# Kernel optimization log

Measured on AMD Instinct MI355X. Metric: run time of the kernel, lower is better.

Reference implementation:

```python
import jax, jax.numpy as jnp
import numpy as np

N = 100000   # nodes
E = 1000000  # edges
DIN = 128    # atom_in_features
DE = 16      # edge_attr_dim
H = 128      # hidden width (preprocess/cheb/postprocess)
K = 3        # Chebyshev order
EPS = 1e-5


def setup_inputs() -> dict:
    key = jax.random.key(0)
    ks = jax.random.split(key, 16)
    s = 0.02
    return {
        "x": jax.random.normal(ks[0], (N, DIN), jnp.float32),
        "edge_index": jax.random.randint(ks[1], (2, E), 0, N),
        "edge_attr": jax.random.normal(ks[2], (E, DE), jnp.float32),
        # AtomEdgeInteraction linear: (DIN+DE) -> H
        "w_int": jax.random.normal(ks[3], (DIN + DE, H), jnp.float32) * s,
        "b_int": jnp.zeros((H,), jnp.float32),
        # preprocess layer 1: Linear + BatchNorm + ReLU
        "w_pre": jax.random.normal(ks[4], (H, H), jnp.float32) * s,
        "b_pre": jnp.zeros((H,), jnp.float32),
        "g_pre": jnp.ones((H,), jnp.float32),
        "be_pre": jnp.zeros((H,), jnp.float32),
        # ChebConv layers: weight [K, in, out] + bias
        "cheb1_w": jax.random.normal(ks[5], (K, H, H), jnp.float32) * s,
        "cheb1_b": jnp.zeros((H,), jnp.float32),
        "cheb2_w": jax.random.normal(ks[6], (K, H, H), jnp.float32) * s,
        "cheb2_b": jnp.zeros((H,), jnp.float32),
        # postprocess: Linear + BatchNorm + ReLU
        "w_post": jax.random.normal(ks[7], (H, H), jnp.float32) * s,
        "b_post": jnp.zeros((H,), jnp.float32),
        "g_post": jnp.ones((H,), jnp.float32),
        "be_post": jnp.zeros((H,), jnp.float32),
        # output layer H -> 1
        "w_out": jax.random.normal(ks[8], (H, 1), jnp.float32) * s,
        "b_out": jnp.zeros((1,), jnp.float32),
    }


def _bn(z, g, b):
    # BatchNorm1d, training-mode batch statistics (biased variance, like torch)
    m = z.mean(0)
    v = ((z - m) ** 2).mean(0)
    return g * (z - m) * jax.lax.rsqrt(v + EPS) + b


def _cheb(h, W, b, row, col, norm):
    # ChebConv with sym normalization, lambda_max=2 => L_hat = -D^{-1/2} A D^{-1/2}
    def lhat(z):
        return jax.ops.segment_sum(norm[:, None] * z[row], col, num_segments=N)

    Tx0 = h
    out = Tx0 @ W[0]
    Tx1 = lhat(Tx0)
    out = out + Tx1 @ W[1]
    for k in range(2, W.shape[0]):
        Tx2 = 2.0 * lhat(Tx1) - Tx0
        out = out + Tx2 @ W[k]
        Tx0, Tx1 = Tx1, Tx2
    return out + b


def reference(x, edge_index, edge_attr,
              w_int, b_int,
              w_pre, b_pre, g_pre, be_pre,
              cheb1_w, cheb1_b, cheb2_w, cheb2_b,
              w_post, b_post, g_post, be_post,
              w_out, b_out):
    row, col = edge_index[0], edge_index[1]
    ones_e = jnp.ones((E,), x.dtype)

    # AtomEdgeInteraction: gather -> concat -> linear -> scatter_mean over col
    comb = jnp.concatenate([x[row], edge_attr], axis=-1)  # [E, DIN+DE]
    upd = comb @ w_int + b_int                             # [E, H]
    cnt = jax.ops.segment_sum(ones_e, col, num_segments=N)
    h = jax.ops.segment_sum(upd, col, num_segments=N) / jnp.clip(cnt, 1.0)[:, None]

    # preprocess layer 1 (Linear + BN + ReLU; dropout rate 0)
    h = jax.nn.relu(_bn(h @ w_pre + b_pre, g_pre, be_pre))

    # sym-normalized edge coefficients for scaled Laplacian
    deg = jax.ops.segment_sum(ones_e, row, num_segments=N)
    dis = jnp.where(deg > 0, jax.lax.rsqrt(jnp.maximum(deg, 1.0)), 0.0)
    norm = -dis[row] * dis[col]  # [E]

    h = jax.nn.relu(_cheb(h, cheb1_w, cheb1_b, row, col, norm))
    h = jax.nn.relu(_cheb(h, cheb2_w, cheb2_b, row, col, norm))

    # postprocess (Linear + BN + ReLU)
    h = jax.nn.relu(_bn(h @ w_post + b_post, g_post, be_post))

    # output layer, squeeze(-1) -> [N]
    return (h @ w_out + b_out).squeeze(-1)
```

## Files before the change

kernel.cpp:

```cpp
#include <hip/hip_runtime.h>
#include <hip/hip_bf16.h>

using u16 = unsigned short;
using u32 = unsigned int;

#define NN 100000
#define NE 1000000
#define NBKT 196
#define NBLK 489

typedef __attribute__((ext_vector_type(8))) short bfrag;
typedef __attribute__((ext_vector_type(4))) float ffrag;

#define BF16ONE2 0x3F803F80u

__device__ __forceinline__ float bf2f(u16 u) { return __uint_as_float(((u32)u) << 16); }
__device__ __forceinline__ u16 f2bf(float f) {
  u32 x = __float_as_uint(f);
  return (u16)((x + 0x7fffu + ((x >> 16) & 1u)) >> 16);
}
__device__ __forceinline__ float rdv(const void* p, long i, int f) {
  return f ? bf2f(((const u16*)p)[i]) : ((const float*)p)[i];
}
__device__ __forceinline__ void acc8(float* a, uint4 v, float w) {
  a[0] = fmaf(w, __uint_as_float(v.x << 16), a[0]);
  a[1] = fmaf(w, __uint_as_float(v.x & 0xffff0000u), a[1]);
  a[2] = fmaf(w, __uint_as_float(v.y << 16), a[2]);
  a[3] = fmaf(w, __uint_as_float(v.y & 0xffff0000u), a[3]);
  a[4] = fmaf(w, __uint_as_float(v.z << 16), a[4]);
  a[5] = fmaf(w, __uint_as_float(v.z & 0xffff0000u), a[5]);
  a[6] = fmaf(w, __uint_as_float(v.w << 16), a[6]);
  a[7] = fmaf(w, __uint_as_float(v.w & 0xffff0000u), a[7]);
}
__device__ __forceinline__ void acc8bn(float* a, uint4 v, float w, const float* A,
                                       const float* Bb) {
  float x;
  x = __uint_as_float(v.x << 16);
  a[0] = fmaf(w, fmaxf(fmaf(A[0], x, Bb[0]), 0.f), a[0]);
  x = __uint_as_float(v.x & 0xffff0000u);
  a[1] = fmaf(w, fmaxf(fmaf(A[1], x, Bb[1]), 0.f), a[1]);
  x = __uint_as_float(v.y << 16);
  a[2] = fmaf(w, fmaxf(fmaf(A[2], x, Bb[2]), 0.f), a[2]);
  x = __uint_as_float(v.y & 0xffff0000u);
  a[3] = fmaf(w, fmaxf(fmaf(A[3], x, Bb[3]), 0.f), a[3]);
  x = __uint_as_float(v.z << 16);
  a[4] = fmaf(w, fmaxf(fmaf(A[4], x, Bb[4]), 0.f), a[4]);
  x = __uint_as_float(v.z & 0xffff0000u);
  a[5] = fmaf(w, fmaxf(fmaf(A[5], x, Bb[5]), 0.f), a[5]);
  x = __uint_as_float(v.w << 16);
  a[6] = fmaf(w, fmaxf(fmaf(A[6], x, Bb[6]), 0.f), a[6]);
  x = __uint_as_float(v.w & 0xffff0000u);
  a[7] = fmaf(w, fmaxf(fmaf(A[7], x, Bb[7]), 0.f), a[7]);
}

#define OWXT 0
#define OWPRE 16384
#define OWD1 32768
#define OW11 49152
#define OV21 65536
#define OWD2 81920
#define OW12 98304
#define OV22 114688
#define OWPOST 131072
#define OWET 147456

#define ASTRIDE 136
#define ESTRIDE 132

struct PrepArgs { const void* in[16]; };

__global__ void k_prep(PrepArgs a, const u32* __restrict__ gp, u16* __restrict__ wq,
                       float* __restrict__ wf) {
  int t = blockIdx.x * 256 + threadIdx.x;
  int f = (gp[0] == BF16ONE2) ? 1 : 0;
  if (t < 16384) {
    int o = t >> 7, k = t & 127;
    int ko = k * 128 + o;
    int ok = o * 128 + k;
    wq[OWXT + ok] = f2bf(rdv(a.in[0], ko, f));
    wq[OWPRE + ok] = f2bf(rdv(a.in[2], ko, f));
    float c0 = rdv(a.in[6], ko, f);
    float c1 = rdv(a.in[6], 16384 + ko, f);
    float c2 = rdv(a.in[6], 32768 + ko, f);
    wq[OWD1 + ok] = f2bf(c0 - c2);
    wq[OW11 + ok] = f2bf(c1);
    wq[OV21 + ok] = f2bf(2.f * c2);
    float d0 = rdv(a.in[8], ko, f);
    float d1 = rdv(a.in[8], 16384 + ko, f);
    float d2 = rdv(a.in[8], 32768 + ko, f);
    wq[OWD2 + ok] = f2bf(d0 - d2);
    wq[OW12 + ok] = f2bf(d1);
    wq[OV22 + ok] = f2bf(2.f * d2);
    wq[OWPOST + ok] = f2bf(rdv(a.in[10], ko, f));
  }
  if (t < 4096) {
    int o = t >> 5, k = t & 31;
    wq[OWET + o * 32 + k] = (k < 16) ? f2bf(rdv(a.in[0], (long)(128 + k) * 128 + o, f)) : (u16)0;
  }
  if (t < 1281) {
    int s = t >> 7, j = t & 127;
    const int map[11] = {1, 3, 4, 5, 7, 9, 11, 12, 13, 14, 15};
    wf[t] = rdv(a.in[map[s]], j, f);
  }
}


__global__ void k_cnt(const int* __restrict__ ei, int* __restrict__ bcnt,
                      int* __restrict__ rbcnt) {
  __shared__ int hc[NBKT], hr[NBKT];
  int t = threadIdx.x, blk = blockIdx.x;
  for (int i = t; i < NBKT; i += 256) { hc[i] = 0; hr[i] = 0; }
  __syncthreads();
  long base = (long)blk * 2048;
#pragma unroll
  for (int i = 0; i < 8; i++) {
    long e = base + i * 256 + t;
    if (e < NE) {
      atomicAdd(&hc[ei[NE + e] >> 9], 1);
      atomicAdd(&hr[ei[e] >> 9], 1);
    }
  }
  __syncthreads();
  for (int i = t; i < NBKT; i += 256) {
    bcnt[i * NBLK + blk] = hc[i];
    rbcnt[i * NBLK + blk] = hr[i];
  }
}

__global__ void k_bscan(int* __restrict__ bcnt, int* __restrict__ rbcnt,
                        int* __restrict__ btot) {
  __shared__ int ss[256];
  int j = blockIdx.x, t = threadIdx.x;
  int* arr = ((j < NBKT) ? bcnt : rbcnt) + (j % NBKT) * NBLK;
  int a = (2 * t < NBLK) ? arr[2 * t] : 0;
  int b = (2 * t + 1 < NBLK) ? arr[2 * t + 1] : 0;
  ss[t] = a + b;
  __syncthreads();
  for (int st = 1; st < 256; st <<= 1) {
    int x = (t >= st) ? ss[t - st] : 0;
    __syncthreads();
    ss[t] += x;
    __syncthreads();
  }
  int base = ss[t] - a - b;
  if (2 * t < NBLK) arr[2 * t] = base;
  if (2 * t + 1 < NBLK) arr[2 * t + 1] = base + a;
  if (t == 255) btot[j] = ss[255];
}

__global__ void k_bbase(const int* __restrict__ btot, int* __restrict__ bbase,
                        int* __restrict__ rbbase, int* __restrict__ off) {
  __shared__ int ss[256];
  int t = threadIdx.x;
  int v = (t < NBKT) ? btot[t] : 0;
  ss[t] = v;
  __syncthreads();
  for (int st = 1; st < 256; st <<= 1) {
    int x = (t >= st) ? ss[t - st] : 0;
    __syncthreads();
    ss[t] += x;
    __syncthreads();
  }
  if (t < NBKT) bbase[t] = ss[t] - v;
  if (t == NBKT - 1) bbase[NBKT] = ss[t];
  __syncthreads();
  int v2 = (t < NBKT) ? btot[NBKT + t] : 0;
  ss[t] = v2;
  __syncthreads();
  for (int st = 1; st < 256; st <<= 1) {
    int x = (t >= st) ? ss[t - st] : 0;
    __syncthreads();
    ss[t] += x;
    __syncthreads();
  }
  if (t < NBKT) rbbase[t] = ss[t] - v2;
  if (t == NBKT - 1) rbbase[NBKT] = ss[t];
  if (t == 0) off[NN] = NE;
}

__global__ void k_scat(const int* __restrict__ ei, const int* __restrict__ bofs,
                       const int* __restrict__ rbofs, const int* __restrict__ bbase,
                       const int* __restrict__ rbbase, u32* __restrict__ sle,
                       u32* __restrict__ srow, u16* __restrict__ srl) {
  __shared__ int cc[NBKT], cr[NBKT], cbase[NBKT], rbase[NBKT];
  int t = threadIdx.x, blk = blockIdx.x;
  for (int i = t; i < NBKT; i += 256) {
    cc[i] = 0;
    cr[i] = 0;
    cbase[i] = bbase[i] + bofs[i * NBLK + blk];
    rbase[i] = rbbase[i] + rbofs[i * NBLK + blk];
  }
  __syncthreads();
  long base = (long)blk * 2048;
#pragma unroll
  for (int i = 0; i < 8; i++) {
    long e = base + i * 256 + t;
    if (e < NE) {
      int c = ei[NE + e], r = ei[e];
      int k1 = atomicAdd(&cc[c >> 9], 1);
      int d1 = cbase[c >> 9] + k1;
      sle[d1] = ((u32)(c & 511) << 20) | (u32)e;
      srow[d1] = (u32)r;
      int k2 = atomicAdd(&cr[r >> 9], 1);
      int d2 = rbase[r >> 9] + k2;
      srl[d2] = (u16)(r & 511);
    }
  }
}

__global__ void k_fine(const u32* __restrict__ sle, const u32* __restrict__ srow,
                       const int* __restrict__ bbase, int* __restrict__ off,
                       int2* __restrict__ cpk) {
  __shared__ u32 hist[512];
  __shared__ u32 ss[256];
  int t = threadIdx.x, b = blockIdx.x;
  hist[t] = 0;
  hist[t + 256] = 0;
  __syncthreads();
  int lo = bbase[b], hi = bbase[b + 1];
  for (int p = lo + t; p < hi; p += 256) atomicAdd(&hist[sle[p] >> 20], 1);
  __syncthreads();
  u32 a = hist[2 * t], bb = hist[2 * t + 1];
  ss[t] = a + bb;
  __syncthreads();
  for (int st = 1; st < 256; st <<= 1) {
    u32 x = (t >= st) ? ss[t - st] : 0;
    __syncthreads();
    ss[t] += x;
    __syncthreads();
  }
  u32 base = ss[t] - a - bb;
  u32 c0 = (u32)lo + base, c1 = (u32)lo + base + a;
  hist[2 * t] = c0;
  hist[2 * t + 1] = c1;
  int col0 = b * 512 + 2 * t, col1 = col0 + 1;
  if (col0 < NN) off[col0] = (int)c0;
  if (col1 < NN) off[col1] = (int)c1;
  __syncthreads();
  for (int p = lo + t; p < hi; p += 256) {
    u32 v = sle[p];
    u32 pos = atomicAdd(&hist[v >> 20], 1);
    cpk[pos] = make_int2((int)srow[p], (int)(v & 0xFFFFFu));
  }
}

__global__ void k_deg(const u16* __restrict__ srl, const int* __restrict__ rbbase,
                      int* __restrict__ deg) {
  __shared__ int hist[512];
  int t = threadIdx.x, b = blockIdx.x;
  hist[t] = 0;
  hist[t + 256] = 0;
  __syncthreads();
  int lo = rbbase[b], hi = rbbase[b + 1];
  for (int p = lo + t; p < hi; p += 256) atomicAdd(&hist[srl[p]], 1);
  __syncthreads();
  int n0 = b * 512 + t, n1 = n0 + 256;
  if (n0 < NN) deg[n0] = hist[t];
  if (n1 < NN) deg[n1] = hist[t + 256];
}

template <int BN>
__global__ __launch_bounds__(256) void k_spmm(const u16* __restrict__ src,
                                              u16* __restrict__ dst,
                                              const int* __restrict__ off,
                                              const int2* __restrict__ cpk,
                                              const float* __restrict__ cnorm,
                                              const float* __restrict__ ab) {
  int t = threadIdx.x;
  int node = blockIdx.x * 8 + (t >> 5);
  if (node >= NN) return;
  int l = t & 31;
  int half = l >> 4;
  int c = (l & 15) * 8;
  float A[8], Bb[8];
  if (BN) {
#pragma unroll
    for (int j = 0; j < 8; j++) {
      A[j] = ab[c + j];
      Bb[j] = ab[128 + c + j];
    }
  }
  int p0 = off[node], p1 = off[node + 1];
  float a[8];
#pragma unroll
  for (int j = 0; j < 8; j++) a[j] = 0.f;
  const u16* sp = src + c;
  for (int p = p0 + half; p < p1; p += 8) {
    int rr[4];
    float w[4];
#pragma unroll
    for (int u = 0; u < 4; u++) {
      int q = p + u * 2;
      int qc = q < p1 ? q : p1 - 1;
      rr[u] = cpk[qc].x;
      w[u] = (q < p1) ? cnorm[qc] : 0.f;
    }
#pragma unroll
    for (int u = 0; u < 4; u++) {
      uint4 v = *(const uint4*)(sp + (long)rr[u] * 128);
      if (BN) acc8bn(a, v, w[u], A, Bb);
      else acc8(a, v, w[u]);
    }
  }
#pragma unroll
  for (int j = 0; j < 8; j++) a[j] += __shfl_xor(a[j], 16);
  if (half) return;
  uint4 o;
  o.x = (u32)f2bf(a[0]) | ((u32)f2bf(a[1]) << 16);
  o.y = (u32)f2bf(a[2]) | ((u32)f2bf(a[3]) << 16);
  o.z = (u32)f2bf(a[4]) | ((u32)f2bf(a[5]) << 16);
  o.w = (u32)f2bf(a[6]) | ((u32)f2bf(a[7]) << 16);
  *(uint4*)(dst + (long)node * 128 + c) = o;
}

template <int WEIGHTED>
__device__ __forceinline__ void gather_lds(u16* sA, const u16* __restrict__ src,
                                           const int* __restrict__ off,
                                           const int2* __restrict__ cpk,
                                           const float* __restrict__ cnorm, int r0) {
  int tid = threadIdx.x;
  int grp = tid >> 4;
  int c = (tid & 15) * 8;
  const u16* sp = src + c;
#pragma unroll
  for (int i = 0; i < 4; i++) {
    int nl = grp * 4 + i;
    int node = r0 + nl;
    float a[8];
#pragma unroll
    for (int j = 0; j < 8; j++) a[j] = 0.f;
    if (node < NN) {
      int p0 = off[node], p1 = off[node + 1];
      for (int p = p0; p < p1; p += 8) {
        int rr[8];
        float w[8];
#pragma unroll
        for (int u = 0; u < 8; u++) {
          int q = p + u;
          int qc = q < p1 ? q : p1 - 1;
          rr[u] = cpk[qc].x;
          w[u] = (q < p1) ? (WEIGHTED ? cnorm[qc] : 1.f) : 0.f;
        }
#pragma unroll
        for (int u = 0; u < 8; u++)
          acc8(a, *(const uint4*)(sp + (long)rr[u] * 128), w[u]);
      }
    }
    uint4 o;
    o.x = (u32)f2bf(a[0]) | ((u32)f2bf(a[1]) << 16);
    o.y = (u32)f2bf(a[2]) | ((u32)f2bf(a[3]) << 16);
    o.z = (u32)f2bf(a[4]) | ((u32)f2bf(a[5]) << 16);
    o.w = (u32)f2bf(a[6]) | ((u32)f2bf(a[7]) << 16);
    *(uint4*)(sA + nl * ASTRIDE + c) = o;
  }
}

__global__ __launch_bounds__(256) void k_asum(const void* __restrict__ eattr,
                                              const u32* __restrict__ gp,
                                              u16* __restrict__ asum,
                                              const int* __restrict__ off,
                                              const int2* __restrict__ cpk,
                                              const int* __restrict__ deg,
                                              float* __restrict__ cnorm) {
  int t = blockIdx.x * 256 + threadIdx.x;
  int node = t >> 4;
  if (node >= NN) return;
  int j = t & 15;
  int p0 = off[node], p1 = off[node + 1];
  int dn = deg[node];
  float ndis = dn > 0 ? -rsqrtf((float)dn) : 0.f;
  for (int p = p0 + j; p < p1; p += 16)
    cnorm[p] = ndis * rsqrtf((float)deg[cpk[p].x]);
  float a = 0.f;
  if (gp[0] == BF16ONE2) {
    const u16* e16 = (const u16*)eattr;
    for (int p = p0; p < p1; p += 8) {
      float s[8];
#pragma unroll
      for (int u = 0; u < 8; u++) {
        int q = p + u;
        int qc = q < p1 ? q : p1 - 1;
        float v = bf2f(e16[(long)cpk[qc].y * 16 + j]);
        s[u] = (q < p1) ? v : 0.f;
      }
      a += ((s[0] + s[1]) + (s[2] + s[3])) + ((s[4] + s[5]) + (s[6] + s[7]));
    }
  } else {
    const float* e32 = (const float*)eattr;
    for (int p = p0; p < p1; p += 8) {
      float s[8];
#pragma unroll
      for (int u = 0; u < 8; u++) {
        int q = p + u;
        int qc = q < p1 ? q : p1 - 1;
        float v = e32[(long)cpk[qc].y * 16 + j];
        s[u] = (q < p1) ? v : 0.f;
      }
      a += ((s[0] + s[1]) + (s[2] + s[3])) + ((s[4] + s[5]) + (s[6] + s[7]));
    }
  }
  asum[(long)node * 16 + j] = f2bf(a);
}

struct MArgs {
  const void* A0; const u16* W0T; int a0raw;
  const float* bias;
  u16* out;
  const u32* gp;
  float* part;
};

__global__ __launch_bounds__(256) void k_mgemm(MArgs m) {
  constexpr int ROWS = 128, RT = 8, TPR = 2, SEGW = 64;
  __shared__ __align__(16) u16 sA[ROWS * ASTRIDE];
  int tid = threadIdx.x;
  int wv = tid >> 6, lane = tid & 63;
  int col16 = lane & 15, quad = lane >> 4;
  int r0 = blockIdx.x * ROWS;

  ffrag acc[RT * 2];
#pragma unroll
  for (int i = 0; i < RT * 2; i++)
#pragma unroll
    for (int g = 0; g < 4; g++) acc[i][g] = 0.f;

  {
    int row = tid / TPR, seg = tid % TPR;
    int ra = r0 + row;
    if (ra >= NN) ra = NN - 1;
    bool f32a = m.a0raw && (m.gp[0] != BF16ONE2);
    if (f32a) {
      const float* gs = (const float*)m.A0 + (long)ra * 128 + seg * SEGW;
      u32* lp = (u32*)(sA + row * ASTRIDE + seg * SEGW);
#pragma unroll
      for (int e = 0; e < SEGW / 8; e++) {
        float4 v0 = *(const float4*)(gs + e * 8);
        float4 v1 = *(const float4*)(gs + e * 8 + 4);
        lp[e * 4 + 0] = (u32)f2bf(v0.x) | ((u32)f2bf(v0.y) << 16);
        lp[e * 4 + 1] = (u32)f2bf(v0.z) | ((u32)f2bf(v0.w) << 16);
        lp[e * 4 + 2] = (u32)f2bf(v1.x) | ((u32)f2bf(v1.y) << 16);
        lp[e * 4 + 3] = (u32)f2bf(v1.z) | ((u32)f2bf(v1.w) << 16);
      }
    } else {
      const u16* gs = (const u16*)m.A0 + (long)ra * 128 + seg * SEGW;
      uint4* lp = (uint4*)(sA + row * ASTRIDE + seg * SEGW);
#pragma unroll
      for (int e = 0; e < SEGW / 8; e++) lp[e] = *(const uint4*)(gs + e * 8);
    }
  }
  bfrag b0[2][4];
#pragma unroll
  for (int c = 0; c < 2; c++)
#pragma unroll
    for (int kb = 0; kb < 4; kb++)
      b0[c][kb] = *(const bfrag*)(m.W0T + (long)(wv * 32 + c * 16 + col16) * 128 + kb * 32 + quad * 8);
  __syncthreads();
#pragma unroll
  for (int kb = 0; kb < 4; kb++)
#pragma unroll
    for (int rt = 0; rt < RT; rt++) {
      bfrag af = *(const bfrag*)(sA + (rt * 16 + col16) * ASTRIDE + kb * 32 + quad * 8);
      acc[rt * 2 + 0] = __builtin_amdgcn_mfma_f32_16x16x32_bf16(af, b0[0][kb], acc[rt * 2 + 0], 0, 0, 0);
      acc[rt * 2 + 1] = __builtin_amdgcn_mfma_f32_16x16x32_bf16(af, b0[1][kb], acc[rt * 2 + 1], 0, 0, 0);
    }
  __syncthreads();
#pragma unroll
  for (int rt = 0; rt < RT; rt++)
#pragma unroll
    for (int c = 0; c < 2; c++) {
      int col = wv * 32 + c * 16 + col16;
      float bj = m.bias ? m.bias[col] : 0.f;
#pragma unroll
      for (int g = 0; g < 4; g++)
        sA[(rt * 16 + quad * 4 + g) * ESTRIDE + col] = f2bf(acc[rt * 2 + c][g] + bj);
    }
  __syncthreads();
  {
    int rr = tid / TPR, d = tid % TPR;
    int rowg = r0 + rr;
    if (rowg < NN) {
      const u16* sp2 = sA + rr * ESTRIDE + d * 64;
      uint4* o = (uint4*)(m.out + (long)rowg * 128 + d * 64);
#pragma unroll
      for (int e = 0; e < 8; e++) {
        const uint2* s2 = (const uint2*)(sp2 + e * 8);
        uint2 lo = s2[0], hi = s2[1];
        o[e] = make_uint4(lo.x, lo.y, hi.x, hi.y);
      }
    }
  }
  if (m.part) {
    __shared__ float ps[256], pq[256];
    int col = tid & 127, hf = tid >> 7;
    float s = 0.f, q = 0.f;
#pragma unroll
    for (int r = 0; r < 64; r++) {
      int rr = hf * 64 + r;
      if (r0 + rr < NN) {
        float v = bf2f(sA[rr * ESTRIDE + col]);
        s += v;
        q += v * v;
      }
    }
    ps[tid] = s;
    pq[tid] = q;
    __syncthreads();
    if (tid < 128) {
      m.part[(long)blockIdx.x * 256 + tid] = ps[tid] + ps[tid + 128];
      m.part[(long)blockIdx.x * 256 + 128 + tid] = pq[tid] + pq[tid + 128];
    }
  }
}

__global__ __launch_bounds__(256) void k_etpre(const u16* __restrict__ Xg,
                                               const u16* __restrict__ asum,
                                               const u16* __restrict__ Wet,
                                               const u16* __restrict__ Wpre,
                                               const float* __restrict__ b_int,
                                               const float* __restrict__ b_pre,
                                               const int* __restrict__ off,
                                               const int2* __restrict__ cpk,
                                               u16* __restrict__ out, float* part) {
  __shared__ __align__(16) u16 sA[64 * ASTRIDE];
  __shared__ __align__(16) u16 sE[64 * 32];
  int tid = threadIdx.x;
  int wv = tid >> 6, lane = tid & 63;
  int col16 = lane & 15, quad = lane >> 4;
  int r0 = blockIdx.x * 64;

  gather_lds<0>(sA, Xg, off, cpk, nullptr, r0);
  {
    int row = tid >> 2, seg = tid & 3;
    int ra = r0 + row;
    if (ra >= NN) ra = NN - 1;
    if (seg < 2)
      *(uint4*)(sE + row * 32 + seg * 8) = *(const uint4*)(asum + (long)ra * 16 + seg * 8);
    else
      *(uint4*)(sE + row * 32 + seg * 8) = make_uint4(0, 0, 0, 0);
  }
  bfrag be[2];
#pragma unroll
  for (int c = 0; c < 2; c++)
    be[c] = *(const bfrag*)(Wet + (long)(wv * 32 + c * 16 + col16) * 32 + quad * 8);
  __syncthreads();
  ffrag accE[8];
#pragma unroll
  for (int i = 0; i < 8; i++)
#pragma unroll
    for (int g = 0; g < 4; g++) accE[i][g] = 0.f;
#pragma unroll
  for (int rt = 0; rt < 4; rt++) {
    bfrag af = *(const bfrag*)(sE + (rt * 16 + col16) * 32 + quad * 8);
    accE[rt * 2 + 0] = __builtin_amdgcn_mfma_f32_16x16x32_bf16(af, be[0], accE[rt * 2 + 0], 0, 0, 0);
    accE[rt * 2 + 1] = __builtin_amdgcn_mfma_f32_16x16x32_bf16(af, be[1], accE[rt * 2 + 1], 0, 0, 0);
  }
#pragma unroll
  for (int rt = 0; rt < 4; rt++)
#pragma unroll
    for (int g = 0; g < 4; g++) {
      int rr = rt * 16 + quad * 4 + g;
      int r = r0 + rr;
      int cc = (r < NN) ? off[r + 1] - off[r] : 0;
      float inv = 1.f / (float)(cc > 1 ? cc : 1);
#pragma unroll
      for (int c = 0; c < 2; c++) {
        int col = wv * 32 + c * 16 + col16;
        float bj = b_int[col];
        float v = accE[rt * 2 + c][g] + bf2f(sA[rr * ASTRIDE + col]);
        v = (v + (float)cc * bj) * inv;
        sA[rr * ASTRIDE + col] = f2bf(v);
      }
    }
  bfrag b1[2][4];
#pragma unroll
  for (int c = 0; c < 2; c++)
#pragma unroll
    for (int kb = 0; kb < 4; kb++)
      b1[c][kb] = *(const bfrag*)(Wpre + (long)(wv * 32 + c * 16 + col16) * 128 + kb * 32 + quad * 8);
  __syncthreads();
  ffrag a2[8];
#pragma unroll
  for (int i = 0; i < 8; i++)
#pragma unroll
    for (int g = 0; g < 4; g++) a2[i][g] = 0.f;
#pragma unroll
  for (int kb = 0; kb < 4; kb++)
#pragma unroll
    for (int rt = 0; rt < 4; rt++) {
      bfrag af = *(const bfrag*)(sA + (rt * 16 + col16) * ASTRIDE + kb * 32 + quad * 8);
      a2[rt * 2 + 0] = __builtin_amdgcn_mfma_f32_16x16x32_bf16(af, b1[0][kb], a2[rt * 2 + 0], 0, 0, 0);
      a2[rt * 2 + 1] = __builtin_amdgcn_mfma_f32_16x16x32_bf16(af, b1[1][kb], a2[rt * 2 + 1], 0, 0, 0);
    }
  __syncthreads();
#pragma unroll
  for (int rt = 0; rt < 4; rt++)
#pragma unroll
    for (int c = 0; c < 2; c++) {
      int col = wv * 32 + c * 16 + col16;
      float bj = b_pre[col];
#pragma unroll
      for (int g = 0; g < 4; g++)
        sA[(rt * 16 + quad * 4 + g) * ESTRIDE + col] = f2bf(a2[rt * 2 + c][g] + bj);
    }
  __syncthreads();
  {
    int rr = tid >> 2, d = tid & 3;
    int rowg = r0 + rr;
    if (rowg < NN) {
      const u16* sp2 = sA + rr * ESTRIDE + d * 32;
      uint4* o = (uint4*)(out + (long)rowg * 128 + d * 32);
#pragma unroll
      for (int e = 0; e < 4; e++) {
        const uint2* s2 = (const uint2*)(sp2 + e * 8);
        uint2 lo = s2[0], hi = s2[1];
        o[e] = make_uint4(lo.x, lo.y, hi.x, hi.y);
      }
    }
  }
  {
    __shared__ float ps[256], pq[256];
    int col = tid & 127, hf = tid >> 7;
    float s = 0.f, q = 0.f;
#pragma unroll
    for (int r = 0; r < 32; r++) {
      int rr = hf * 32 + r;
      if (r0 + rr < NN) {
        float v = bf2f(sA[rr * ESTRIDE + col]);
        s += v;
        q += v * v;
      }
    }
    ps[tid] = s;
    pq[tid] = q;
    __syncthreads();
    if (tid < 128) {
      part[(long)blockIdx.x * 256 + tid] = ps[tid] + ps[tid + 128];
      part[(long)blockIdx.x * 256 + 128 + tid] = pq[tid] + pq[tid + 128];
    }
  }
}

template <int BN>
__global__ __launch_bounds__(256) void k_cheb(const u16* __restrict__ hb,
                                              const u16* __restrict__ T1,
                                              const int* __restrict__ off,
                                              const int2* __restrict__ cpk,
                                              const float* __restrict__ cnorm,
                                              const u16* __restrict__ WD,
                                              const u16* __restrict__ W1,
                                              const u16* __restrict__ V2,
                                              const float* __restrict__ bias,
                                              const float* __restrict__ ab,
                                              u16* __restrict__ out) {
  __shared__ __align__(16) u16 sA[64 * ASTRIDE];
  int tid = threadIdx.x;
  int wv = tid >> 6, lane = tid & 63;
  int col16 = lane & 15, quad = lane >> 4;
  int r0 = blockIdx.x * 64;

  gather_lds<1>(sA, T1, off, cpk, cnorm, r0);
  bfrag bv[2][4];
#pragma unroll
  for (int c = 0; c < 2; c++)
#pragma unroll
    for (int kb = 0; kb < 4; kb++)
      bv[c][kb] = *(const bfrag*)(V2 + (long)(wv * 32 + c * 16 + col16) * 128 + kb * 32 + quad * 8);
  __syncthreads();
  ffrag acc[8];
#pragma unroll
  for (int i = 0; i < 8; i++)
#pragma unroll
    for (int g = 0; g < 4; g++) acc[i][g] = 0.f;
#pragma unroll
  for (int kb = 0; kb < 4; kb++)
#pragma unroll
    for (int rt = 0; rt < 4; rt++) {
      bfrag af = *(const bfrag*)(sA + (rt * 16 + col16) * ASTRIDE + kb * 32 + quad * 8);
      acc[rt * 2 + 0] = __builtin_amdgcn_mfma_f32_16x16x32_bf16(af, bv[0][kb], acc[rt * 2 + 0], 0, 0, 0);
      acc[rt * 2 + 1] = __builtin_amdgcn_mfma_f32_16x16x32_bf16(af, bv[1][kb], acc[rt * 2 + 1], 0, 0, 0);
    }
  __syncthreads();

  {
    int row = tid >> 2, seg = tid & 3;
    int ra = r0 + row;
    if (ra >= NN) ra = NN - 1;
    const u16* gs = hb + (long)ra * 128 + seg * 32;
    uint4* lp = (uint4*)(sA + row * ASTRIDE + seg * 32);
    if (BN) {
#pragma unroll
      for (int e = 0; e < 4; e++) {
        uint4 v = *(const uint4*)(gs + e * 8);
        int cb = seg * 32 + e * 8;
        float f0 = fmaxf(fmaf(ab[cb + 0], __uint_as_float(v.x << 16), ab[128 + cb + 0]), 0.f);
        float f1 = fmaxf(fmaf(ab[cb + 1], __uint_as_float(v.x & 0xffff0000u), ab[128 + cb + 1]), 0.f);
        float f2 = fmaxf(fmaf(ab[cb + 2], __uint_as_float(v.y << 16), ab[128 + cb + 2]), 0.f);
        float f3 = fmaxf(fmaf(ab[cb + 3], __uint_as_float(v.y & 0xffff0000u), ab[128 + cb + 3]), 0.f);
        float f4 = fmaxf(fmaf(ab[cb + 4], __uint_as_float(v.z << 16), ab[128 + cb + 4]), 0.f);
        float f5 = fmaxf(fmaf(ab[cb + 5], __uint_as_float(v.z & 0xffff0000u), ab[128 + cb + 5]), 0.f);
        float f6 = fmaxf(fmaf(ab[cb + 6], __uint_as_float(v.w << 16), ab[128 + cb + 6]), 0.f);
        float f7 = fmaxf(fmaf(ab[cb + 7], __uint_as_float(v.w & 0xffff0000u), ab[128 + cb + 7]), 0.f);
        uint4 o;
        o.x = (u32)f2bf(f0) | ((u32)f2bf(f1) << 16);
        o.y = (u32)f2bf(f2) | ((u32)f2bf(f3) << 16);
        o.z = (u32)f2bf(f4) | ((u32)f2bf(f5) << 16);
        o.w = (u32)f2bf(f6) | ((u32)f2bf(f7) << 16);
        lp[e] = o;
      }
    } else {
#pragma unroll
      for (int e = 0; e < 4; e++) lp[e] = *(const uint4*)(gs + e * 8);
    }
  }
#pragma unroll
  for (int c = 0; c < 2; c++)
#pragma unroll
    for (int kb = 0; kb < 4; kb++)
      bv[c][kb] = *(const bfrag*)(WD + (long)(wv * 32 + c * 16 + col16) * 128 + kb * 32 + quad * 8);
  __syncthreads();
#pragma unroll
  for (int kb = 0; kb < 4; kb++)
#pragma unroll
    for (int rt = 0; rt < 4; rt++) {
      bfrag af = *(const bfrag*)(sA + (rt * 16 + col16) * ASTRIDE + kb * 32 + quad * 8);
      acc[rt * 2 + 0] = __builtin_amdgcn_mfma_f32_16x16x32_bf16(af, bv[0][kb], acc[rt * 2 + 0], 0, 0, 0);
      acc[rt * 2 + 1] = __builtin_amdgcn_mfma_f32_16x16x32_bf16(af, bv[1][kb], acc[rt * 2 + 1], 0, 0, 0);
    }
  __syncthreads();

  {
    int row = tid >> 2, seg = tid & 3;
    int ra = r0 + row;
    if (ra >= NN) ra = NN - 1;
    const u16* gs = T1 + (long)ra * 128 + seg * 32;
    uint4* lp = (uint4*)(sA + row * ASTRIDE + seg * 32);
#pragma unroll
    for (int e = 0; e < 4; e++) lp[e] = *(const uint4*)(gs + e * 8);
  }
#pragma unroll
  for (int c = 0; c < 2; c++)
#pragma unroll
    for (int kb = 0; kb < 4; kb++)
      bv[c][kb] = *(const bfrag*)(W1 + (long)(wv * 32 + c * 16 + col16) * 128 + kb * 32 + quad * 8);
  __syncthreads();
#pragma unroll
  for (int kb = 0; kb < 4; kb++)
#pragma unroll
    for (int rt = 0; rt < 4; rt++) {
      bfrag af = *(const bfrag*)(sA + (rt * 16 + col16) * ASTRIDE + kb * 32 + quad * 8);
      acc[rt * 2 + 0] = __builtin_amdgcn_mfma_f32_16x16x32_bf16(af, bv[0][kb], acc[rt * 2 + 0], 0, 0, 0);
      acc[rt * 2 + 1] = __builtin_amdgcn_mfma_f32_16x16x32_bf16(af, bv[1][kb], acc[rt * 2 + 1], 0, 0, 0);
    }
  __syncthreads();

#pragma unroll
  for (int rt = 0; rt < 4; rt++)
#pragma unroll
    for (int c = 0; c < 2; c++) {
      int col = wv * 32 + c * 16 + col16;
      float bj = bias[col];
#pragma unroll
      for (int g = 0; g < 4; g++)
        sA[(rt * 16 + quad * 4 + g) * ESTRIDE + col] = f2bf(fmaxf(acc[rt * 2 + c][g] + bj, 0.f));
    }
  __syncthreads();
  {
    int rr = tid >> 2, d = tid & 3;
    int rowg = r0 + rr;
    if (rowg < NN) {
      const u16* sp2 = sA + rr * ESTRIDE + d * 32;
      uint4* o = (uint4*)(out + (long)rowg * 128 + d * 32);
#pragma unroll
      for (int e = 0; e < 4; e++) {
        const uint2* s2 = (const uint2*)(sp2 + e * 8);
        uint2 lo = s2[0], hi = s2[1];
        o[e] = make_uint4(lo.x, lo.y, hi.x, hi.y);
      }
    }
  }
}

__global__ void k_redfin(const float* __restrict__ part, const float* __restrict__ gamma,
                         const float* __restrict__ beta, float* ab, int nblk) {
  int tid = threadIdx.x;
  int col = blockIdx.x * 16 + (tid & 15);
  int ch = tid >> 4;
  float s = 0.f, q = 0.f;
  for (int b = ch; b < nblk; b += 16) {
    s += part[(long)b * 256 + col];
    q += part[(long)b * 256 + 128 + col];
  }
  __shared__ float sh[256], qh[256];
  sh[tid] = s;
  qh[tid] = q;
  __syncthreads();
  if (tid < 16) {
    float ts = 0.f, tq = 0.f;
#pragma unroll
    for (int i = 0; i < 16; i++) {
      ts += sh[i * 16 + tid];
      tq += qh[i * 16 + tid];
    }
    int j = blockIdx.x * 16 + tid;
    float m = ts * (1.f / (float)NN);
    float v = fmaxf(tq * (1.f / (float)NN) - m * m, 0.f);
    float a = gamma[j] * rsqrtf(v + 1e-5f);
    ab[j] = a;
    ab[128 + j] = beta[j] - m * a;
  }
}

__global__ void k_out(const u16* __restrict__ z, const float* __restrict__ ab,
                      const float* __restrict__ wout, const float* __restrict__ bout,
                      const u32* __restrict__ gp, void* __restrict__ y) {
  int node = blockIdx.x * 4 + (threadIdx.x >> 6);
  if (node >= NN) return;
  int lane = threadIdx.x & 63;
  float s = 0.f;
#pragma unroll
  for (int c = lane; c < 128; c += 64) {
    float zz = bf2f(z[(long)node * 128 + c]);
    float h = fmaxf(ab[c] * zz + ab[128 + c], 0.f);
    s += h * wout[c];
  }
#pragma unroll
  for (int o = 32; o > 0; o >>= 1) s += __shfl_down(s, o);
  if (lane == 0) {
    float r = s + bout[0];
    if (gp[0] == BF16ONE2) ((u16*)y)[node] = f2bf(r);
    else ((float*)y)[node] = r;
  }
}

extern "C" void kernel_launch(void* const* d_in, const int* in_sizes, int n_in,
                              void* d_out, int out_size, void* d_ws, size_t ws_size,
                              hipStream_t stream) {
  const void* x = d_in[0];
  const int* ei = (const int*)d_in[1];
  const void* eattr = d_in[2];
  const u32* gp = (const u32*)d_in[7];
  (void)in_sizes; (void)n_in; (void)out_size; (void)ws_size;

  char* w = (char*)d_ws;
  size_t p = 0;
  auto alloc = [&](size_t b) { size_t r = p; p += (b + 255) & ~(size_t)255; return r; };
  size_t o_deg = alloc((size_t)NN * 4);
  size_t o_off = alloc((size_t)(NN + 1) * 4);
  size_t o_bcnt = alloc((size_t)NBKT * NBLK * 4);
  size_t o_rbcnt = alloc((size_t)NBKT * NBLK * 4);
  size_t o_btot = alloc((size_t)2 * NBKT * 4);
  size_t o_bbase = alloc((size_t)(NBKT + 1) * 4);
  size_t o_rbbase = alloc((size_t)(NBKT + 1) * 4);
  size_t o_ab = alloc(512 * 4);
  size_t o_wq = alloc((size_t)151552 * 2);
  size_t o_wf = alloc((size_t)1281 * 4);
  size_t o_cpk = alloc((size_t)NE * 8);
  size_t o_cnrm = alloc((size_t)NE * 4);
  size_t o_asum = alloc((size_t)NN * 16 * 2);
  size_t o_part = alloc((size_t)1563 * 256 * 4);
  size_t o_Bx = alloc((size_t)NN * 128 * 2);
  size_t o_Bt = alloc((size_t)NN * 128 * 2);

  int* deg = (int*)(w + o_deg);
  int* off = (int*)(w + o_off);
  int* bcnt = (int*)(w + o_bcnt);
  int* rbcnt = (int*)(w + o_rbcnt);
  int* btot = (int*)(w + o_btot);
  int* bbase = (int*)(w + o_bbase);
  int* rbbase = (int*)(w + o_rbbase);
  float* abA = (float*)(w + o_ab);
  float* abB = abA + 256;
  u16* wq = (u16*)(w + o_wq);
  float* wf = (float*)(w + o_wf);
  int2* cpk = (int2*)(w + o_cpk);
  float* cnrm = (float*)(w + o_cnrm);
  u16* asum = (u16*)(w + o_asum);
  float* part = (float*)(w + o_part);
  u16* Bx = (u16*)(w + o_Bx);
  u16* Bt = (u16*)(w + o_Bt);
  u32* sle = (u32*)Bx;
  u32* srow = sle + NE;
  u16* srl = (u16*)(srow + NE);

  int gS = (NN + 7) / 8;
  int gG1 = (NN + 127) / 128;
  int gG2 = (NN + 63) / 64;

  {
    PrepArgs a;
    for (int i = 0; i < 16; i++) a.in[i] = d_in[3 + i];
    k_prep<<<64, 256, 0, stream>>>(a, gp, wq, wf);
  }

  k_cnt<<<NBLK, 256, 0, stream>>>(ei, bcnt, rbcnt);
  k_bscan<<<2 * NBKT, 256, 0, stream>>>(bcnt, rbcnt, btot);
  k_bbase<<<1, 256, 0, stream>>>(btot, bbase, rbbase, off);
  k_scat<<<NBLK, 256, 0, stream>>>(ei, bcnt, rbcnt, bbase, rbbase, sle, srow, srl);
  k_fine<<<NBKT, 256, 0, stream>>>(sle, srow, bbase, off, cpk);
  k_deg<<<NBKT, 256, 0, stream>>>(srl, rbbase, deg);

  k_asum<<<(NN * 16 + 255) / 256, 256, 0, stream>>>(eattr, gp, asum, off, cpk, deg, cnrm);

  {
    MArgs a = {};
    a.A0 = x; a.W0T = wq + OWXT; a.a0raw = 1;
    a.out = Bx; a.gp = gp;
    k_mgemm<<<gG1, 256, 0, stream>>>(a);
  }
  k_etpre<<<gG2, 256, 0, stream>>>(Bx, asum, wq + OWET, wq + OWPRE, wf + 0, wf + 128,
                                   off, cpk, Bt, part);
  k_redfin<<<8, 256, 0, stream>>>(part, wf + 256, wf + 384, abA, gG2);

  k_spmm<1><<<gS, 256, 0, stream>>>(Bt, Bx, off, cpk, cnrm, abA);
  k_cheb<1><<<gG2, 256, 0, stream>>>(Bt, Bx, off, cpk, cnrm,
                                     wq + OWD1, wq + OW11, wq + OV21, wf + 512, abA, Bt);

  k_spmm<0><<<gS, 256, 0, stream>>>(Bt, Bx, off, cpk, cnrm, nullptr);
  k_cheb<0><<<gG2, 256, 0, stream>>>(Bt, Bx, off, cpk, cnrm,
                                     wq + OWD2, wq + OW12, wq + OV22, wf + 640, nullptr, Bt);

  {
    MArgs a = {};
    a.A0 = Bt; a.W0T = wq + OWPOST;
    a.bias = wf + 768; a.out = Bx; a.gp = gp; a.part = part;
    k_mgemm<<<gG1, 256, 0, stream>>>(a);
  }
  k_redfin<<<8, 256, 0, stream>>>(part, wf + 896, wf + 1024, abB, gG1);
  k_out<<<(NN + 3) / 4, 256, 0, stream>>>(Bx, abB, wf + 1152, wf + 1280, gp, d_out);
}
```

Before: 671.1 us.

## Split packed CSR into separate row/edge arrays and remap SpMM to 4 lanes per node

Replaces the interleaved int2 CSR entries with separate crow and ceid arrays, so gather paths that only need the source row read half as many index bytes. The SpMM kernel is restructured from 32 lanes per node (two halves combined by a shuffle) to 4 lanes per node, each handling 32 features with four 16-byte loads per neighbor. This removes the cross-lane reduction and raises the number of nodes per block to 64. In exchange each thread holds many more registers (32 accumulators plus 64 BN scale/shift values), which can lower occupancy, and each node's edge loop runs serially with less memory-level parallelism per lane.

```diff
diff --git a/kernel.cpp b/kernel.cpp
--- a/kernel.cpp
+++ b/kernel.cpp
@@ -210,7 +210,7 @@
 
 __global__ void k_fine(const u32* __restrict__ sle, const u32* __restrict__ srow,
                        const int* __restrict__ bbase, int* __restrict__ off,
-                       int2* __restrict__ cpk) {
+                       int* __restrict__ crow, int* __restrict__ ceid) {
   __shared__ u32 hist[512];
   __shared__ u32 ss[256];
   int t = threadIdx.x, b = blockIdx.x;
@@ -240,7 +240,8 @@
   for (int p = lo + t; p < hi; p += 256) {
     u32 v = sle[p];
     u32 pos = atomicAdd(&hist[v >> 20], 1);
-    cpk[pos] = make_int2((int)srow[p], (int)(v & 0xFFFFFu));
+    crow[pos] = (int)srow[p];
+    ceid[pos] = (int)(v & 0xFFFFFu);
   }
 }
 
@@ -260,63 +261,76 @@
 }
 
 template <int BN>
-__global__ __launch_bounds__(256) void k_spmm(const u16* __restrict__ src,
-                                              u16* __restrict__ dst,
-                                              const int* __restrict__ off,
-                                              const int2* __restrict__ cpk,
-                                              const float* __restrict__ cnorm,
-                                              const float* __restrict__ ab) {
-  int t = threadIdx.x;
-  int node = blockIdx.x * 8 + (t >> 5);
+__global__ __launch_bounds__(256) void k_spmm4(const u16* __restrict__ src,
+                                               u16* __restrict__ dst,
+                                               const int* __restrict__ off,
+                                               const int* __restrict__ crow,
+                                               const float* __restrict__ cnorm,
+                                               const float* __restrict__ ab) {
+  int tid = threadIdx.x;
+  int node = blockIdx.x * 64 + (tid >> 2);
   if (node >= NN) return;
-  int l = t & 31;
-  int half = l >> 4;
-  int c = (l & 15) * 8;
-  float A[8], Bb[8];
+  int ln = tid & 3;
+  int c = ln * 32;
+  float A[32], Bb[32];
   if (BN) {
 #pragma unroll
-    for (int j = 0; j < 8; j++) {
+    for (int j = 0; j < 32; j++) {
       A[j] = ab[c + j];
       Bb[j] = ab[128 + c + j];
     }
   }
   int p0 = off[node], p1 = off[node + 1];
-  float a[8];
-#pragma unroll
-  for (int j = 0; j < 8; j++) a[j] = 0.f;
+  float a[32];
+#pragma unroll
+  for (int j = 0; j < 32; j++) a[j] = 0.f;
   const u16* sp = src + c;
-  for (int p = p0 + half; p < p1; p += 8) {
+  for (int p = p0; p < p1; p += 4) {
     int rr[4];
     float w[4];
 #pragma unroll
     for (int u = 0; u < 4; u++) {
-      int q = p + u * 2;
+      int q = p + u;
       int qc = q < p1 ? q : p1 - 1;
-      rr[u] = cpk[qc].x;
+      rr[u] = crow[qc];
       w[u] = (q < p1) ? cnorm[qc] : 0.f;
     }
 #pragma unroll
     for (int u = 0; u < 4; u++) {
-      uint4 v = *(const uint4*)(sp + (long)rr[u] * 128);
-      if (BN) acc8bn(a, v, w[u], A, Bb);
-      else acc8(a, v, w[u]);
-    }
-  }
-#pragma unroll
-  for (int j = 0; j < 8; j++) a[j] += __shfl_xor(a[j], 16);
-  if (half) return;
-  uint4 o;
-  o.x = (u32)f2bf(a[0]) | ((u32)f2bf(a[1]) << 16);
-  o.y = (u32)f2bf(a[2]) | ((u32)f2bf(a[3]) << 16);
-  o.z = (u32)f2bf(a[4]) | ((u32)f2bf(a[5]) << 16);
-  o.w = (u32)f2bf(a[6]) | ((u32)f2bf(a[7]) << 16);
-  *(uint4*)(dst + (long)node * 128 + c) = o;
+      const u16* rp = sp + (long)rr[u] * 128;
+      uint4 v0 = *(const uint4*)(rp);
+      uint4 v1 = *(const uint4*)(rp + 8);
+      uint4 v2 = *(const uint4*)(rp + 16);
+      uint4 v3 = *(const uint4*)(rp + 24);
+      if (BN) {
+        acc8bn(a + 0, v0, w[u], A + 0, Bb + 0);
+        acc8bn(a + 8, v1, w[u], A + 8, Bb + 8);
+        acc8bn(a + 16, v2, w[u], A + 16, Bb + 16);
+        acc8bn(a + 24, v3, w[u], A + 24, Bb + 24);
+      } else {
+        acc8(a + 0, v0, w[u]);
+        acc8(a + 8, v1, w[u]);
+        acc8(a + 16, v2, w[u]);
+        acc8(a + 24, v3, w[u]);
+      }
+    }
+  }
+  uint4* d = (uint4*)(dst + (long)node * 128 + c);
+#pragma unroll
+  for (int e = 0; e < 4; e++) {
+    uint4 o;
+    o.x = (u32)f2bf(a[e * 8 + 0]) | ((u32)f2bf(a[e * 8 + 1]) << 16);
+    o.y = (u32)f2bf(a[e * 8 + 2]) | ((u32)f2bf(a[e * 8 + 3]) << 16);
+    o.z = (u32)f2bf(a[e * 8 + 4]) | ((u32)f2bf(a[e * 8 + 5]) << 16);
+    o.w = (u32)f2bf(a[e * 8 + 6]) | ((u32)f2bf(a[e * 8 + 7]) << 16);
+    d[e] = o;
+  }
 }
 
 template <int WEIGHTED>
 __device__ __forceinline__ void gather_lds(u16* sA, const u16* __restrict__ src,
                                            const int* __restrict__ off,
-                                           const int2* __restrict__ cpk,
+                                           const int* __restrict__ crow,
                                            const float* __restrict__ cnorm, int r0) {
   int tid = threadIdx.x;
   int grp = tid >> 4;
@@ -338,7 +352,7 @@
         for (int u = 0; u < 8; u++) {
           int q = p + u;
           int qc = q < p1 ? q : p1 - 1;
-          rr[u] = cpk[qc].x;
+          rr[u] = crow[qc];
           w[u] = (q < p1) ? (WEIGHTED ? cnorm[qc] : 1.f) : 0.f;
         }
 #pragma unroll
@@ -359,7 +373,8 @@
                                               const u32* __restrict__ gp,
                                               u16* __restrict__ asum,
                                               const int* __restrict__ off,
-                                              const int2* __restrict__ cpk,
+                                              const int* __restrict__ ceid,
+                                              const int* __restrict__ crow,
                                               const int* __restrict__ deg,
                                               float* __restrict__ cnorm) {
   int t = blockIdx.x * 256 + threadIdx.x;
@@ -370,33 +385,33 @@
   int dn = deg[node];
   float ndis = dn > 0 ? -rsqrtf((float)dn) : 0.f;
   for (int p = p0 + j; p < p1; p += 16)
-    cnorm[p] = ndis * rsqrtf((float)deg[cpk[p].x]);
+    cnorm[p] = ndis * rsqrtf((float)deg[crow[p]]);
   float a = 0.f;
   if (gp[0] == BF16ONE2) {
     const u16* e16 = (const u16*)eattr;
     for (int p = p0; p < p1; p += 8) {
-      float s[8];
+      float s8[8];
 #pragma unroll
       for (int u = 0; u < 8; u++) {
         int q = p + u;
         int qc = q < p1 ? q : p1 - 1;
-        float v = bf2f(e16[(long)cpk[qc].y * 16 + j]);
-        s[u] = (q < p1) ? v : 0.f;
-      }
-      a += ((s[0] + s[1]) + (s[2] + s[3])) + ((s[4] + s[5]) + (s[6] + s[7]));
+        float v = bf2f(e16[(long)ceid[qc] * 16 + j]);
+        s8[u] = (q < p1) ? v : 0.f;
+      }
+      a += ((s8[0] + s8[1]) + (s8[2] + s8[3])) + ((s8[4] + s8[5]) + (s8[6] + s8[7]));
     }
   } else {
     const float* e32 = (const float*)eattr;
     for (int p = p0; p < p1; p += 8) {
-      float s[8];
+      float s8[8];
 #pragma unroll
       for (int u = 0; u < 8; u++) {
         int q = p + u;
         int qc = q < p1 ? q : p1 - 1;
-        float v = e32[(long)cpk[qc].y * 16 + j];
-        s[u] = (q < p1) ? v : 0.f;
-      }
-      a += ((s[0] + s[1]) + (s[2] + s[3])) + ((s[4] + s[5]) + (s[6] + s[7]));
+        float v = e32[(long)ceid[qc] * 16 + j];
+        s8[u] = (q < p1) ? v : 0.f;
+      }
+      a += ((s8[0] + s8[1]) + (s8[2] + s8[3])) + ((s8[4] + s8[5]) + (s8[6] + s8[7]));
     }
   }
   asum[(long)node * 16 + j] = f2bf(a);
@@ -519,7 +534,7 @@
                                                const float* __restrict__ b_int,
                                                const float* __restrict__ b_pre,
                                                const int* __restrict__ off,
-                                               const int2* __restrict__ cpk,
+                                               const int* __restrict__ crow,
                                                u16* __restrict__ out, float* part) {
   __shared__ __align__(16) u16 sA[64 * ASTRIDE];
   __shared__ __align__(16) u16 sE[64 * 32];
@@ -528,7 +543,7 @@
   int col16 = lane & 15, quad = lane >> 4;
   int r0 = blockIdx.x * 64;
 
-  gather_lds<0>(sA, Xg, off, cpk, nullptr, r0);
+  gather_lds<0>(sA, Xg, off, crow, nullptr, r0);
   {
     int row = tid >> 2, seg = tid & 3;
     int ra = r0 + row;
@@ -644,7 +659,7 @@
 __global__ __launch_bounds__(256) void k_cheb(const u16* __restrict__ hb,
                                               const u16* __restrict__ T1,
                                               const int* __restrict__ off,
-                                              const int2* __restrict__ cpk,
+                                              const int* __restrict__ crow,
                                               const float* __restrict__ cnorm,
                                               const u16* __restrict__ WD,
                                               const u16* __restrict__ W1,
@@ -658,7 +673,7 @@
   int col16 = lane & 15, quad = lane >> 4;
   int r0 = blockIdx.x * 64;
 
-  gather_lds<1>(sA, T1, off, cpk, cnorm, r0);
+  gather_lds<1>(sA, T1, off, crow, cnorm, r0);
   bfrag bv[2][4];
 #pragma unroll
   for (int c = 0; c < 2; c++)
@@ -854,7 +869,8 @@
   size_t o_ab = alloc(512 * 4);
   size_t o_wq = alloc((size_t)151552 * 2);
   size_t o_wf = alloc((size_t)1281 * 4);
-  size_t o_cpk = alloc((size_t)NE * 8);
+  size_t o_crow = alloc((size_t)NE * 4);
+  size_t o_ceid = alloc((size_t)NE * 4);
   size_t o_cnrm = alloc((size_t)NE * 4);
   size_t o_asum = alloc((size_t)NN * 16 * 2);
   size_t o_part = alloc((size_t)1563 * 256 * 4);
@@ -872,7 +888,8 @@
   float* abB = abA + 256;
   u16* wq = (u16*)(w + o_wq);
   float* wf = (float*)(w + o_wf);
-  int2* cpk = (int2*)(w + o_cpk);
+  int* crow = (int*)(w + o_crow);
+  int* ceid = (int*)(w + o_ceid);
   float* cnrm = (float*)(w + o_cnrm);
   u16* asum = (u16*)(w + o_asum);
   float* part = (float*)(w + o_part);
@@ -882,7 +899,7 @@
   u32* srow = sle + NE;
   u16* srl = (u16*)(srow + NE);
 
-  int gS = (NN + 7) / 8;
+  int gN16 = (NN * 16 + 255) / 256;
   int gG1 = (NN + 127) / 128;
   int gG2 = (NN + 63) / 64;
 
@@ -896,10 +913,10 @@
   k_bscan<<<2 * NBKT, 256, 0, stream>>>(bcnt, rbcnt, btot);
   k_bbase<<<1, 256, 0, stream>>>(btot, bbase, rbbase, off);
   k_scat<<<NBLK, 256, 0, stream>>>(ei, bcnt, rbcnt, bbase, rbbase, sle, srow, srl);
-  k_fine<<<NBKT, 256, 0, stream>>>(sle, srow, bbase, off, cpk);
+  k_fine<<<NBKT, 256, 0, stream>>>(sle, srow, bbase, off, crow, ceid);
   k_deg<<<NBKT, 256, 0, stream>>>(srl, rbbase, deg);
 
-  k_asum<<<(NN * 16 + 255) / 256, 256, 0, stream>>>(eattr, gp, asum, off, cpk, deg, cnrm);
+  k_asum<<<gN16, 256, 0, stream>>>(eattr, gp, asum, off, ceid, crow, deg, cnrm);
 
   {
     MArgs a = {};
@@ -908,15 +925,15 @@
     k_mgemm<<<gG1, 256, 0, stream>>>(a);
   }
   k_etpre<<<gG2, 256, 0, stream>>>(Bx, asum, wq + OWET, wq + OWPRE, wf + 0, wf + 128,
-                                   off, cpk, Bt, part);
+                                   off, crow, Bt, part);
   k_redfin<<<8, 256, 0, stream>>>(part, wf + 256, wf + 384, abA, gG2);
 
-  k_spmm<1><<<gS, 256, 0, stream>>>(Bt, Bx, off, cpk, cnrm, abA);
-  k_cheb<1><<<gG2, 256, 0, stream>>>(Bt, Bx, off, cpk, cnrm,
+  k_spmm4<1><<<gG2, 256, 0, stream>>>(Bt, Bx, off, crow, cnrm, abA);
+  k_cheb<1><<<gG2, 256, 0, stream>>>(Bt, Bx, off, crow, cnrm,
                                      wq + OWD1, wq + OW11, wq + OV21, wf + 512, abA, Bt);
 
-  k_spmm<0><<<gS, 256, 0, stream>>>(Bt, Bx, off, cpk, cnrm, nullptr);
-  k_cheb<0><<<gG2, 256, 0, stream>>>(Bt, Bx, off, cpk, cnrm,
+  k_spmm4<0><<<gG2, 256, 0, stream>>>(Bt, Bx, off, crow, cnrm, nullptr);
+  k_cheb<0><<<gG2, 256, 0, stream>>>(Bt, Bx, off, crow, cnrm,
                                      wq + OWD2, wq + OW12, wq + OV22, wf + 640, nullptr, Bt);
 
   {
```

New measurement: 698.6 us. 1.04x slower.
